# Optimization experiments

Measured on AMD Instinct MI355X. Metric: run time of the kernel, lower is better.

## Reference

```python
import jax, jax.numpy as jnp
import numpy as np

DIM = 1536
NH = 12
HD = DIM // NH          # 128
C = HD // 2             # 64 complex freq slots per head
DT = C - 2 * (C // 3)   # 22 temporal
DS = C // 3             # 21 per spatial axis
EPS = 1e-6
M_TAB = 64              # rope table length (>= max(f,h,w))


def _rope_tables():
    def tab(d):
        inv = 1.0 / (10000.0 ** (np.arange(d, dtype=np.float64) / d))
        ang = np.outer(np.arange(M_TAB, dtype=np.float64), inv)
        return np.cos(ang), np.sin(ang)
    ct, st = tab(DT)
    ch, sh = tab(DS)
    cw, sw = tab(DS)
    fc = np.concatenate([ct, ch, cw], axis=1).astype(np.float32)  # [M, 64]
    fs = np.concatenate([st, sh, sw], axis=1).astype(np.float32)
    return jnp.asarray(fc), jnp.asarray(fs)


def setup_inputs() -> dict:
    key = jax.random.key(0)
    ks = jax.random.split(key, 6)
    B, F, H, W = 1, 8, 22, 40
    L = F * H * W  # 7040
    s = 0.02
    x = jax.random.normal(ks[0], (B, L, DIM), jnp.float32)
    Wq = jax.random.normal(ks[1], (DIM, DIM), jnp.float32) * s
    Wk = jax.random.normal(ks[2], (DIM, DIM), jnp.float32) * s
    Wv = jax.random.normal(ks[3], (DIM, DIM), jnp.float32) * s
    Wo = jax.random.normal(ks[4], (DIM, DIM), jnp.float32) * s
    bk2 = jax.random.split(ks[5], 4)
    bq = jax.random.normal(bk2[0], (DIM,), jnp.float32) * s
    bk = jax.random.normal(bk2[1], (DIM,), jnp.float32) * s
    bv = jax.random.normal(bk2[2], (DIM,), jnp.float32) * s
    bo = jax.random.normal(bk2[3], (DIM,), jnp.float32) * s
    fc, fs = _rope_tables()
    return dict(x=x, Wq=Wq, bq=bq, Wk=Wk, bk=bk, Wv=Wv, bv=bv, Wo=Wo, bo=bo,
                gq=jnp.ones((DIM,), jnp.float32), gk=jnp.ones((DIM,), jnp.float32),
                freqs_cos=fc, freqs_sin=fs,
                num_frames=F, grid_h=H, grid_w=W,
                chunk_size=2, sink_size=1, max_attention_size=2640)


def _pos_table(tab, f, h, w):
    # tab: [M, 64] -> per-token [f*h*w, 64] via (t,h,w) axis split [22,21,21]
    t = jnp.broadcast_to(tab[:f, :DT][:, None, None, :], (f, h, w, DT))
    hh = jnp.broadcast_to(tab[:h, DT:DT + DS][None, :, None, :], (f, h, w, DS))
    ww = jnp.broadcast_to(tab[:w, DT + DS:][None, None, :, :], (f, h, w, DS))
    return jnp.concatenate([t, hh, ww], axis=-1).reshape(f * h * w, C)


def _forward(x, Wq, bq, Wk, bk, Wv, bv, Wo, bo, gq, gk, freqs_cos, freqs_sin,
             num_frames, grid_h, grid_w, chunk_size, sink_size, max_attention_size):
    B, L, D = x.shape
    lin = lambda t, W, b: jnp.einsum('bld,ed->ble', t, W) + b
    rms = lambda t, g: t * jax.lax.rsqrt(jnp.mean(t * t, axis=-1, keepdims=True) + EPS) * g

    q = rms(lin(x, Wq, bq), gq).reshape(B, L, NH, HD)
    k = rms(lin(x, Wk, bk), gk).reshape(B, L, NH, HD)
    v = lin(x, Wv, bv).reshape(B, L, NH, HD)

    # causal RoPE (start_frame=0)
    cosL = _pos_table(freqs_cos, num_frames, grid_h, grid_w)  # [L, 64]
    sinL = _pos_table(freqs_sin, num_frames, grid_h, grid_w)

    def rope(t):
        a = t.reshape(B, L, NH, C, 2)
        xr, xi = a[..., 0], a[..., 1]
        co = cosL[None, :, None, :]
        si = sinL[None, :, None, :]
        return jnp.stack([xr * co - xi * si, xr * si + xi * co], axis=-1).reshape(B, L, NH, HD)

    q = rope(q)
    k = rope(k)

    # loop attention, diffusion forcing: chunk i attends [0,(i+1)*block) with sink+window
    frame_seqlen = grid_h * grid_w
    block = frame_seqlen * chunk_size
    total_len = num_frames * frame_seqlen
    sink_end = sink_size * frame_seqlen
    num_chunks = -(-total_len // block)
    scale = 1.0 / (HD ** 0.5)

    def attn(qi, ki, vi):
        s = jnp.einsum('bqnd,bknd->bnqk', qi, ki) * scale
        p = jax.nn.softmax(s, axis=-1)
        return jnp.einsum('bnqk,bknd->bqnd', p, vi)

    outs = []
    for i in range(num_chunks):
        q_start = i * block
        q_end = min((i + 1) * block, total_len)
        qi = q[:, q_start:q_end]
        chunk_end = q_end
        if max_attention_size == -1 or sink_end == 0:
            if max_attention_size == -1:
                ki, vi = k[:, :chunk_end], v[:, :chunk_end]
            else:
                ws = max(0, chunk_end - max_attention_size)
                ki, vi = k[:, ws:chunk_end], v[:, ws:chunk_end]
        else:
            window = max_attention_size - sink_end
            ws = max(sink_end, chunk_end - window)
            ki = jnp.concatenate([k[:, :sink_end], k[:, ws:chunk_end]], axis=1)
            vi = jnp.concatenate([v[:, :sink_end], v[:, ws:chunk_end]], axis=1)
        outs.append(attn(qi, ki, vi))

    o = jnp.concatenate(outs, axis=1).reshape(B, L, D)
    return jnp.einsum('bld,ed->ble', o, Wo) + bo


def reference(x, Wq, bq, Wk, bk, Wv, bv, Wo, bo, gq, gk, freqs_cos, freqs_sin,
              num_frames, grid_h, grid_w, chunk_size, sink_size, max_attention_size):
    return _forward(x, Wq, bq, Wk, bk, Wv, bv, Wo, bo, gq, gk, freqs_cos, freqs_sin,
                    num_frames, grid_h, grid_w, chunk_size, sink_size, max_attention_size)
```

## Files before the change

kernel.cpp:

```cpp
#include <hip/hip_runtime.h>
#include <math.h>

typedef __attribute__((ext_vector_type(8))) short short8;
typedef __attribute__((ext_vector_type(4))) float f32x4;
typedef __attribute__((ext_vector_type(16))) float f32x16;
typedef __attribute__((ext_vector_type(4))) float f4;
typedef __attribute__((ext_vector_type(4))) unsigned short us4;
typedef __attribute__((ext_vector_type(2))) unsigned int u32x2;

#define MFMA16(a,b,c) __builtin_amdgcn_mfma_f32_16x16x32_bf16(a,b,c,0,0,0)
#define MFMA32(a,b,c) __builtin_amdgcn_mfma_f32_32x32x16_bf16(a,b,c,0,0,0)

__device__ __forceinline__ unsigned short f2bf(float f) {
  unsigned int u = __float_as_uint(f);
  u = (u + 0x7FFFu + ((u >> 16) & 1u)) >> 16;
  return (unsigned short)u;
}
__device__ __forceinline__ float bf2f(unsigned short b) {
  return __uint_as_float(((unsigned int)b) << 16);
}
__device__ __forceinline__ unsigned int pk2(float a, float b) {
  unsigned int au = __float_as_uint(a) + 0x8000u;
  unsigned int bu = __float_as_uint(b) + 0x8000u;
  return __builtin_amdgcn_perm(bu, au, 0x07060302u);
}

typedef const __attribute__((address_space(1))) unsigned int* gas_t;
typedef __attribute__((address_space(3))) unsigned int* las_t;
__device__ __forceinline__ void gl16(const void* g, void* l) {
  __builtin_amdgcn_global_load_lds((gas_t)g, (las_t)l, 16, 0, 0);
}

__global__ void cvt_f32_bf16(const float* __restrict__ in,
                             unsigned short* __restrict__ out, int n4) {
  int i = blockIdx.x * blockDim.x + threadIdx.x;
  const int stride = gridDim.x * blockDim.x;
  for (; i < n4; i += stride) {
    f4 v = ((const f4*)in)[i];
    us4 o;
    o[0] = f2bf(v[0]); o[1] = f2bf(v[1]); o[2] = f2bf(v[2]); o[3] = f2bf(v[3]);
    ((us4*)out)[i] = o;
  }
}

template<int F32OUT>
__global__ __launch_bounds__(256)
void gemm_bt(const unsigned short* __restrict__ A,
             const unsigned short* __restrict__ B,
             const float* __restrict__ bias,
             unsigned short* __restrict__ obf,
             float* __restrict__ of32,
             int K, int ldo)
{
  const int tid = threadIdx.x;
  const int wave = tid >> 6, lane = tid & 63, lg = lane >> 4, lr = lane & 15;
  const int wr = wave >> 1, wc = wave & 1;
  const int m0 = blockIdx.y * 128, n0 = blockIdx.x * 128;

  __shared__ __align__(16) unsigned short Al[128 * 32];
  __shared__ __align__(16) unsigned short Bl[128 * 32];

  f32x4 acc[4][4];
#pragma unroll
  for (int m = 0; m < 4; ++m)
#pragma unroll
    for (int n = 0; n < 4; ++n) acc[m][n] = (f32x4){0.f, 0.f, 0.f, 0.f};

  const int r0 = tid >> 2, r1 = (tid + 256) >> 2;
  const int c0 = (tid & 3) * 8;
  const long arow0 = (long)(m0 + r0) * K, arow1 = (long)(m0 + r1) * K;
  const long brow0 = (long)(n0 + r0) * K, brow1 = (long)(n0 + r1) * K;

  for (int k0 = 0; k0 < K; k0 += 32) {
    gl16(A + arow0 + k0 + c0, (char*)Al + tid * 16);
    gl16(A + arow1 + k0 + c0, (char*)Al + (tid + 256) * 16);
    gl16(B + brow0 + k0 + c0, (char*)Bl + tid * 16);
    gl16(B + brow1 + k0 + c0, (char*)Bl + (tid + 256) * 16);
    __syncthreads();
    short8 af[4], bf[4];
#pragma unroll
    for (int m = 0; m < 4; ++m)
      af[m] = *(const short8*)(Al + (wr * 64 + m * 16 + lr) * 32 + lg * 8);
#pragma unroll
    for (int n = 0; n < 4; ++n)
      bf[n] = *(const short8*)(Bl + (wc * 64 + n * 16 + lr) * 32 + lg * 8);
#pragma unroll
    for (int m = 0; m < 4; ++m)
#pragma unroll
      for (int n = 0; n < 4; ++n)
        acc[m][n] = MFMA16(af[m], bf[n], acc[m][n]);
    __syncthreads();
  }

#pragma unroll
  for (int n = 0; n < 4; ++n) {
    const int col = n0 + wc * 64 + n * 16 + lr;
    const float bs = bias[col];
#pragma unroll
    for (int m = 0; m < 4; ++m) {
      const int row = m0 + wr * 64 + m * 16 + lg * 4;
#pragma unroll
      for (int r = 0; r < 4; ++r) {
        float v = acc[m][n][r] + bs;
        if (F32OUT) of32[(long)(row + r) * ldo + col] = v;
        else        obf[(long)(row + r) * ldo + col] = f2bf(v);
      }
    }
  }
}

__global__ __launch_bounds__(256)
void normrope(unsigned short* __restrict__ qkv, const float* __restrict__ g,
              const float* __restrict__ fc, const float* __restrict__ fs,
              int colOff, float oscale)
{
  const int l = blockIdx.x, tid = threadIdx.x;
  __shared__ float rowbuf[1536];
  __shared__ float sred[4];
  unsigned short* rp = qkv + (long)l * 4608 + colOff;

  float ss = 0.f;
  if (tid < 192) {
    short8 v = *(const short8*)(rp + tid * 8);
#pragma unroll
    for (int e = 0; e < 8; ++e) {
      float f = bf2f((unsigned short)v[e]);
      rowbuf[tid * 8 + e] = f;
      ss += f * f;
    }
  }
#pragma unroll
  for (int m = 32; m; m >>= 1) ss += __shfl_xor(ss, m, 64);
  if ((tid & 63) == 0) sred[tid >> 6] = ss;
  __syncthreads();
  const float rs = rsqrtf((sred[0] + sred[1] + sred[2] + sred[3]) * (1.f / 1536.f) + 1e-6f);

  const int f_ = l / 880, rem = l % 880, h_ = rem / 40, w_ = rem % 40;
#pragma unroll
  for (int j = 0; j < 3; ++j) {
    int p = tid + j * 256;
    int head = p >> 6, c = p & 63;
    int e = head * 128 + 2 * c;
    int tr = (c < 22) ? f_ : ((c < 43) ? h_ : w_);
    float co = fc[tr * 64 + c], si = fs[tr * 64 + c];
    float xr = rowbuf[e] * rs * g[e];
    float xi = rowbuf[e + 1] * rs * g[e + 1];
    float yr = (xr * co - xi * si) * oscale;
    float yi = (xr * si + xi * co) * oscale;
    unsigned int pk = (unsigned int)f2bf(yr) | ((unsigned int)f2bf(yi) << 16);
    *(unsigned int*)(rp + e) = pk;
  }
}

__device__ __forceinline__ void issueK(const unsigned short* __restrict__ qkv,
                                       int h, int t, int kvlen, int woff, int tid,
                                       unsigned short* Kbuf)
{
#pragma unroll
  for (int i = 0; i < 4; ++i) {
    int s = i * 256 + tid;
    int kvl = s >> 4;
    int dc = (s & 15) ^ (kvl & 7);
    int j = t * 64 + kvl; j = j < kvlen ? j : kvlen - 1;
    int gk = j + (j >= 880 ? woff : 0);
    gl16(qkv + (long)gk * 4608 + 1536 + h * 128 + dc * 8, (char*)Kbuf + s * 16);
  }
}

__device__ __forceinline__ void loadV(const unsigned short* __restrict__ qkv,
                                      int h, int t, int kvlen, int woff, int tid,
                                      short8 vp[2][2])
{
#pragma unroll
  for (int i = 0; i < 2; ++i) {
    int task = i * 256 + tid;
    int dc = task & 15, kp = task >> 4;
    int kvl = kp * 2;
    int j0 = t * 64 + kvl, j1 = j0 + 1;
    j0 = j0 < kvlen ? j0 : kvlen - 1;
    j1 = j1 < kvlen ? j1 : kvlen - 1;
    int g0 = j0 + (j0 >= 880 ? woff : 0);
    int g1 = j1 + (j1 >= 880 ? woff : 0);
    vp[i][0] = *(const short8*)(qkv + (long)g0 * 4608 + 3072 + h * 128 + dc * 8);
    vp[i][1] = *(const short8*)(qkv + (long)g1 * 4608 + 3072 + h * 128 + dc * 8);
  }
}

__device__ __forceinline__ void writeV(int tid, short8 vp[2][2], unsigned short* Vt)
{
#pragma unroll
  for (int i = 0; i < 2; ++i) {
    int task = i * 256 + tid;
    int dc = task & 15, kp = task >> 4;
    int kvl = kp * 2;
#pragma unroll
    for (int e = 0; e < 8; ++e) {
      int d = dc * 8 + e;
      int byte = d * 128 + kvl * 2;
      byte ^= (((d & 7) ^ ((d >> 3) & 7)) << 4);
      *(unsigned int*)((char*)Vt + byte) =
          (unsigned int)(unsigned short)vp[i][0][e] |
          ((unsigned int)(unsigned short)vp[i][1][e] << 16);
    }
  }
}

__global__ __launch_bounds__(256, 2)
void attn_kern(const unsigned short* __restrict__ qkv,
               unsigned short* __restrict__ ob)
{
  const int qt = blockIdx.x, ci = blockIdx.y, h = blockIdx.z;
  const int tid = threadIdx.x, wave = tid >> 6, lane = tid & 63;
  const int l31 = lane & 31, hh = lane >> 5;
  const int chunk_start = ci * 1760, chunk_end = chunk_start + 1760;
  const int wstart = (ci == 0) ? 880 : ci * 1760;
  const int woff = wstart - 880;
  const int kvlen = 880 + (chunk_end - wstart);
  const int q0 = chunk_start + qt * 128;

  __shared__ __align__(16) unsigned short Kl[2][64 * 128];
  __shared__ __align__(16) unsigned short Vt[2][128 * 64];

  int qr = q0 + wave * 32 + l31;
  if (qr >= chunk_end) qr = chunk_end - 1;
  const unsigned short* qp = qkv + (long)qr * 4608 + h * 128;
  short8 qf[8];
#pragma unroll
  for (int st = 0; st < 8; ++st) qf[st] = *(const short8*)(qp + st * 16 + hh * 8);

  f32x16 Oc[4];
#pragma unroll
  for (int i = 0; i < 4; ++i)
#pragma unroll
    for (int j = 0; j < 16; ++j) Oc[i][j] = 0.f;
  float m_run = -1e30f, l_run = 0.f;

  const int nt = (kvlen + 63) >> 6;
  short8 vp[2][2];
  issueK(qkv, h, 0, kvlen, woff, tid, &Kl[0][0]);
  loadV(qkv, h, 0, kvlen, woff, tid, vp);
  writeV(tid, vp, &Vt[0][0]);
  __syncthreads();

  for (int t = 0; t < nt; ++t) {
    const int cur = t & 1;
    const bool pf = (t + 1 < nt);
    if (pf) {
      issueK(qkv, h, t + 1, kvlen, woff, tid, &Kl[cur ^ 1][0]);
      loadV(qkv, h, t + 1, kvlen, woff, tid, vp);
    }

    f32x16 s0, s1;
#pragma unroll
    for (int j = 0; j < 16; ++j) { s0[j] = 0.f; s1[j] = 0.f; }
    __builtin_amdgcn_s_setprio(1);
#pragma unroll
    for (int st = 0; st < 8; ++st) {
      int off = 32 * st + 16 * hh;
      int b0 = l31 * 256 + (off ^ ((l31 & 7) << 4));
      short8 k0 = *(const short8*)((const char*)&Kl[cur][0] + b0);
      s0 = MFMA32(k0, qf[st], s0);
      int b1 = (32 + l31) * 256 + (off ^ ((l31 & 7) << 4));
      short8 k1 = *(const short8*)((const char*)&Kl[cur][0] + b1);
      s1 = MFMA32(k1, qf[st], s1);
    }
    __builtin_amdgcn_s_setprio(0);

    if (t * 64 + 64 > kvlen) {
#pragma unroll
      for (int r = 0; r < 16; ++r) {
        int kv0 = t * 64 + (r & 3) + 8 * (r >> 2) + 4 * hh;
        if (kv0 >= kvlen)      s0[r] = -1e30f;
        if (kv0 + 32 >= kvlen) s1[r] = -1e30f;
      }
    }

    float mx[16];
#pragma unroll
    for (int r = 0; r < 16; ++r) mx[r] = fmaxf(s0[r], s1[r]);
#pragma unroll
    for (int w = 8; w; w >>= 1)
#pragma unroll
      for (int r = 0; r < w; ++r) mx[r] = fmaxf(mx[r], mx[r + w]);
    float pm = fmaxf(mx[0], __shfl_xor(mx[0], 32, 64));

    const bool defer = __all(pm <= m_run + 8.f);
    const float mn = defer ? m_run : fmaxf(m_run, pm);

#pragma unroll
    for (int r = 0; r < 16; ++r) {
      s0[r] = __builtin_amdgcn_exp2f(s0[r] - mn);
      s1[r] = __builtin_amdgcn_exp2f(s1[r] - mn);
    }
    float sm[16];
#pragma unroll
    for (int r = 0; r < 16; ++r) sm[r] = s0[r] + s1[r];
#pragma unroll
    for (int w = 8; w; w >>= 1)
#pragma unroll
      for (int r = 0; r < w; ++r) sm[r] += sm[r + w];
    float sum = sm[0] + __shfl_xor(sm[0], 32, 64);

    if (defer) {
      l_run += sum;
    } else {
      float al = __builtin_amdgcn_exp2f(m_run - mn);
      l_run = l_run * al + sum;
      m_run = mn;
#pragma unroll
      for (int i = 0; i < 4; ++i)
#pragma unroll
        for (int j = 0; j < 16; ++j) Oc[i][j] *= al;
    }

    unsigned int w0[8], w1[8];
#pragma unroll
    for (int m = 0; m < 8; ++m) {
      w0[m] = pk2(s0[2 * m], s0[2 * m + 1]);
      w1[m] = pk2(s1[2 * m], s1[2 * m + 1]);
    }

    if (pf) writeV(tid, vp, &Vt[cur ^ 1][0]);

    __builtin_amdgcn_s_setprio(1);
#pragma unroll
    for (int s = 0; s < 4; ++s) {
      const unsigned int* w = (s < 2) ? w0 : w1;
      const int lo4 = (s & 1) * 4;
      unsigned int x0 = __shfl_xor(w[lo4 + 2], 32, 64);
      unsigned int x1 = __shfl_xor(w[lo4 + 3], 32, 64);
      unsigned int y0 = __shfl_xor(w[lo4],     32, 64);
      unsigned int y1 = __shfl_xor(w[lo4 + 1], 32, 64);
      unsigned int fw[4];
      fw[0] = hh ? x0 : w[lo4];
      fw[1] = hh ? x1 : w[lo4 + 1];
      fw[2] = hh ? w[lo4 + 2] : y0;
      fw[3] = hh ? w[lo4 + 3] : y1;
      short8 pb = *(const short8*)fw;
#pragma unroll
      for (int dt = 0; dt < 4; ++dt) {
        int d = dt * 32 + l31;
        int byte = d * 128 + s * 32 + hh * 16;
        byte ^= (((d & 7) ^ ((d >> 3) & 7)) << 4);
        short8 vf = *(const short8*)((const char*)&Vt[cur][0] + byte);
        Oc[dt] = MFMA32(vf, pb, Oc[dt]);
      }
    }
    __builtin_amdgcn_s_setprio(0);

    __syncthreads();
  }

  const int qg = q0 + wave * 32 + l31;
  if (qg < chunk_end) {
    const float inv = 1.f / l_run;
    unsigned short* op = ob + (long)qg * 1536 + h * 128;
#pragma unroll
    for (int dt = 0; dt < 4; ++dt) {
#pragma unroll
      for (int gblk = 0; gblk < 4; ++gblk) {
        int d = dt * 32 + gblk * 8 + hh * 4;
        unsigned int u0 = pk2(Oc[dt][4 * gblk]     * inv, Oc[dt][4 * gblk + 1] * inv);
        unsigned int u1 = pk2(Oc[dt][4 * gblk + 2] * inv, Oc[dt][4 * gblk + 3] * inv);
        u32x2 uu; uu[0] = u0; uu[1] = u1;
        *(u32x2*)(op + d) = uu;
      }
    }
  }
}

extern "C" void kernel_launch(void* const* d_in, const int* in_sizes, int n_in,
                              void* d_out, int out_size, void* d_ws, size_t ws_size,
                              hipStream_t stream)
{
  const float* x  = (const float*)d_in[0];
  const float* Wq = (const float*)d_in[1];
  const float* bq = (const float*)d_in[2];
  const float* Wk = (const float*)d_in[3];
  const float* bk = (const float*)d_in[4];
  const float* Wv = (const float*)d_in[5];
  const float* bv = (const float*)d_in[6];
  const float* Wo = (const float*)d_in[7];
  const float* bo = (const float*)d_in[8];
  const float* gq = (const float*)d_in[9];
  const float* gk = (const float*)d_in[10];
  const float* fc = (const float*)d_in[11];
  const float* fs = (const float*)d_in[12];

  char* ws = (char*)d_ws;
  unsigned short* xb   = (unsigned short*)(ws);
  unsigned short* wcat = (unsigned short*)(ws + 21626880);
  unsigned short* wob  = (unsigned short*)(ws + 35782656);
  float*          bcat = (float*)(ws + 40501248);
  unsigned short* qkv  = (unsigned short*)(ws + 40519680);
  unsigned short* obuf = (unsigned short*)(ws + 105400320);

  cvt_f32_bf16<<<2048, 256, 0, stream>>>(x,  xb,   10813440 / 4);
  cvt_f32_bf16<<<1024, 256, 0, stream>>>(Wq, wcat,            2359296 / 4);
  cvt_f32_bf16<<<1024, 256, 0, stream>>>(Wk, wcat + 2359296,  2359296 / 4);
  cvt_f32_bf16<<<1024, 256, 0, stream>>>(Wv, wcat + 4718592,  2359296 / 4);
  cvt_f32_bf16<<<1024, 256, 0, stream>>>(Wo, wob,             2359296 / 4);
  hipMemcpyAsync(bcat,        bq, 1536 * 4, hipMemcpyDeviceToDevice, stream);
  hipMemcpyAsync(bcat + 1536, bk, 1536 * 4, hipMemcpyDeviceToDevice, stream);
  hipMemcpyAsync(bcat + 3072, bv, 1536 * 4, hipMemcpyDeviceToDevice, stream);

  gemm_bt<0><<<dim3(36, 55), 256, 0, stream>>>(xb, wcat, bcat, qkv, nullptr, 1536, 4608);

  const float qsc = (float)(1.4426950408889634 / sqrt(128.0));
  normrope<<<7040, 256, 0, stream>>>(qkv, gq, fc, fs, 0,    qsc);
  normrope<<<7040, 256, 0, stream>>>(qkv, gk, fc, fs, 1536, 1.0f);

  attn_kern<<<dim3(14, 4, 12), 256, 0, stream>>>(qkv, obuf);

  gemm_bt<1><<<dim3(12, 55), 256, 0, stream>>>(obuf, wob, bo, nullptr, (float*)d_out, 1536, 1536);
}
```

Measured before the change: 449.2 us.

## Software-pipeline attention loop: overlap next tile's QK MFMAs with current softmax

Restructures the flash-attention KV loop so the QK^T scores for tile t+1 are computed before the softmax and PV of tile t. K is prefetched two tiles ahead into the double buffer. The goal is to let MFMA work for the next tile overlap with the exp/reduction VALU work of the current one and hide load latency. In exchange it keeps an extra pair of 16-float score accumulators live, which raises register pressure and may reduce occupancy.

```diff
diff --git a/kernel.cpp b/kernel.cpp
--- a/kernel.cpp
+++ b/kernel.cpp
@@ -234,73 +234,59 @@
 #pragma unroll
     for (int j = 0; j < 16; ++j) Oc[i][j] = 0.f;
   float m_run = -1e30f, l_run = 0.f;
-
-  const int nt = (kvlen + 63) >> 6;
-  short8 vp[2][2];
-  issueK(qkv, h, 0, kvlen, woff, tid, &Kl[0][0]);
-  loadV(qkv, h, 0, kvlen, woff, tid, vp);
-  writeV(tid, vp, &Vt[0][0]);
-  __syncthreads();
-
-  for (int t = 0; t < nt; ++t) {
-    const int cur = t & 1;
-    const bool pf = (t + 1 < nt);
-    if (pf) {
-      issueK(qkv, h, t + 1, kvlen, woff, tid, &Kl[cur ^ 1][0]);
-      loadV(qkv, h, t + 1, kvlen, woff, tid, vp);
-    }
-
-    f32x16 s0, s1;
-#pragma unroll
-    for (int j = 0; j < 16; ++j) { s0[j] = 0.f; s1[j] = 0.f; }
+  unsigned int w0[8], w1[8];
+
+  auto computeQK = [&](int t, int cur, f32x16* S0, f32x16* S1) {
+    f32x16 a0, a1;
+#pragma unroll
+    for (int j = 0; j < 16; ++j) { a0[j] = 0.f; a1[j] = 0.f; }
     __builtin_amdgcn_s_setprio(1);
 #pragma unroll
     for (int st = 0; st < 8; ++st) {
       int off = 32 * st + 16 * hh;
       int b0 = l31 * 256 + (off ^ ((l31 & 7) << 4));
       short8 k0 = *(const short8*)((const char*)&Kl[cur][0] + b0);
-      s0 = MFMA32(k0, qf[st], s0);
+      a0 = MFMA32(k0, qf[st], a0);
       int b1 = (32 + l31) * 256 + (off ^ ((l31 & 7) << 4));
       short8 k1 = *(const short8*)((const char*)&Kl[cur][0] + b1);
-      s1 = MFMA32(k1, qf[st], s1);
+      a1 = MFMA32(k1, qf[st], a1);
     }
     __builtin_amdgcn_s_setprio(0);
-
     if (t * 64 + 64 > kvlen) {
 #pragma unroll
       for (int r = 0; r < 16; ++r) {
         int kv0 = t * 64 + (r & 3) + 8 * (r >> 2) + 4 * hh;
-        if (kv0 >= kvlen)      s0[r] = -1e30f;
-        if (kv0 + 32 >= kvlen) s1[r] = -1e30f;
+        if (kv0 >= kvlen)      a0[r] = -1e30f;
+        if (kv0 + 32 >= kvlen) a1[r] = -1e30f;
       }
     }
-
+    *S0 = a0; *S1 = a1;
+  };
+
+  auto finishTile = [&](f32x16& s0f, f32x16& s1f) {
     float mx[16];
 #pragma unroll
-    for (int r = 0; r < 16; ++r) mx[r] = fmaxf(s0[r], s1[r]);
+    for (int r = 0; r < 16; ++r) mx[r] = fmaxf(s0f[r], s1f[r]);
 #pragma unroll
     for (int w = 8; w; w >>= 1)
 #pragma unroll
       for (int r = 0; r < w; ++r) mx[r] = fmaxf(mx[r], mx[r + w]);
     float pm = fmaxf(mx[0], __shfl_xor(mx[0], 32, 64));
-
     const bool defer = __all(pm <= m_run + 8.f);
     const float mn = defer ? m_run : fmaxf(m_run, pm);
-
 #pragma unroll
     for (int r = 0; r < 16; ++r) {
-      s0[r] = __builtin_amdgcn_exp2f(s0[r] - mn);
-      s1[r] = __builtin_amdgcn_exp2f(s1[r] - mn);
+      s0f[r] = __builtin_amdgcn_exp2f(s0f[r] - mn);
+      s1f[r] = __builtin_amdgcn_exp2f(s1f[r] - mn);
     }
     float sm[16];
 #pragma unroll
-    for (int r = 0; r < 16; ++r) sm[r] = s0[r] + s1[r];
+    for (int r = 0; r < 16; ++r) sm[r] = s0f[r] + s1f[r];
 #pragma unroll
     for (int w = 8; w; w >>= 1)
 #pragma unroll
       for (int r = 0; r < w; ++r) sm[r] += sm[r + w];
     float sum = sm[0] + __shfl_xor(sm[0], 32, 64);
-
     if (defer) {
       l_run += sum;
     } else {
@@ -312,16 +298,14 @@
 #pragma unroll
         for (int j = 0; j < 16; ++j) Oc[i][j] *= al;
     }
-
-    unsigned int w0[8], w1[8];
 #pragma unroll
     for (int m = 0; m < 8; ++m) {
-      w0[m] = pk2(s0[2 * m], s0[2 * m + 1]);
-      w1[m] = pk2(s1[2 * m], s1[2 * m + 1]);
-    }
-
-    if (pf) writeV(tid, vp, &Vt[cur ^ 1][0]);
-
+      w0[m] = pk2(s0f[2 * m], s0f[2 * m + 1]);
+      w1[m] = pk2(s1f[2 * m], s1f[2 * m + 1]);
+    }
+  };
+
+  auto doPV = [&](int cur) {
     __builtin_amdgcn_s_setprio(1);
 #pragma unroll
     for (int s = 0; s < 4; ++s) {
@@ -347,9 +331,36 @@
       }
     }
     __builtin_amdgcn_s_setprio(0);
-
+  };
+
+  const int nt = (kvlen + 63) >> 6;
+  short8 vp[2][2];
+
+  issueK(qkv, h, 0, kvlen, woff, tid, &Kl[0][0]);
+  if (nt > 1) issueK(qkv, h, 1, kvlen, woff, tid, &Kl[1][0]);
+  loadV(qkv, h, 0, kvlen, woff, tid, vp);
+  writeV(tid, vp, &Vt[0][0]);
+  __syncthreads();
+
+  f32x16 sp0, sp1;
+  computeQK(0, 0, &sp0, &sp1);
+  __syncthreads();
+
+  for (int t = 0; t < nt - 1; ++t) {
+    const int cur = t & 1;
+    if (t + 2 < nt) issueK(qkv, h, t + 2, kvlen, woff, tid, &Kl[cur][0]);
+    loadV(qkv, h, t + 1, kvlen, woff, tid, vp);
+
+    f32x16 sc0, sc1;
+    computeQK(t + 1, cur ^ 1, &sc0, &sc1);
+    finishTile(sp0, sp1);
+    writeV(tid, vp, &Vt[cur ^ 1][0]);
+    doPV(cur);
     __syncthreads();
-  }
+    sp0 = sc0; sp1 = sc1;
+  }
+  finishTile(sp0, sp1);
+  doPV((nt - 1) & 1);
 
   const int qg = q0 + wave * 32 + l31;
   if (qg < chunk_end) {
```

New measurement: 442.5 us. About the same (-1.5%).
